# Kernel tuning notes

Hardware: AMD Instinct MI355X
Metric: run time of the kernel (lower is better)

The kernel has to match this reference:

```python
import jax, jax.numpy as jnp
import numpy as np

BN_EPS = 1e-5
DIM = 256
RED = 4
KH, KW = 3, 3


def setup_inputs() -> dict:
    key = jax.random.key(0)
    ks = jax.random.split(key, 4)
    b, c, h, w = 32, DIM, 64, 64
    hid = DIM // RED
    x = jax.random.normal(ks[0], (b, c, h, w), dtype=jnp.float32)
    # 1x1 convs are just matmuls on pooled [b, c] vectors; store as [out, in]
    w1 = jax.random.normal(ks[1], (hid, c), dtype=jnp.float32) * (1.0 / np.sqrt(c))
    bn_gamma = jnp.ones((hid,), dtype=jnp.float32)
    bn_beta = jnp.zeros((hid,), dtype=jnp.float32)
    bn_mean = jnp.zeros((hid,), dtype=jnp.float32)
    bn_var = jnp.ones((hid,), dtype=jnp.float32)
    w2 = jax.random.normal(ks[2], (c * KH * KW, hid), dtype=jnp.float32) * (1.0 / np.sqrt(hid))
    b2 = jnp.zeros((c * KH * KW,), dtype=jnp.float32)
    bias = jnp.zeros((c,), dtype=jnp.float32)
    return {"x": x, "w1": w1, "bn_gamma": bn_gamma, "bn_beta": bn_beta,
            "bn_mean": bn_mean, "bn_var": bn_var, "w2": w2, "b2": b2, "bias": bias}


def reference(x, w1, bn_gamma, bn_beta, bn_mean, bn_var, w2, b2, bias):
    b, c, h, w = x.shape
    # --- SE-style dynamic weight generation ---
    pooled = jnp.mean(x, axis=(2, 3))                      # [b, c]
    y = jnp.einsum('bc,rc->br', pooled, w1)                # conv1 (1x1, no bias)
    y = (y - bn_mean) * jax.lax.rsqrt(bn_var + BN_EPS) * bn_gamma + bn_beta
    y = jax.nn.sigmoid(y)                                  # note: relu is defined but unused in forward
    dyn = jnp.einsum('br,kr->bk', y, w2) + b2              # [b, c*KH*KW]
    dyn = dyn.reshape(b * c, 1, KH, KW)                    # per-sample depthwise kernels (OIHW)
    # --- per-sample depthwise conv via batch-as-groups trick ---
    out = jax.lax.conv_general_dilated(
        x.reshape(1, b * c, h, w), dyn,
        window_strides=(1, 1), padding=((1, 1), (1, 1)),
        feature_group_count=b * c,
        dimension_numbers=('NCHW', 'OIHW', 'NCHW'))
    out = out.reshape(b, c, h, w) + bias[None, :, None, None]
    return out
```

## Files before the change

kernel.cpp:

```cpp
#include <hip/hip_runtime.h>
#include <hip/hip_bf16.h>

#define DIM 256
#define HID 64
#define HW 4096
#define KK 2304
#define LW 73

__global__ __launch_bounds__(256) void pool_kernel(const float* __restrict__ x,
                                                   float* __restrict__ pooled) {
    int plane = blockIdx.x;
    const float4* p = (const float4*)(x + (size_t)plane * HW);
    int tid = threadIdx.x;
    float s = 0.f;
#pragma unroll
    for (int k = 0; k < 4; ++k) {
        float4 v = p[tid + k * 256];
        s += (v.x + v.y) + (v.z + v.w);
    }
#pragma unroll
    for (int off = 32; off > 0; off >>= 1) s += __shfl_down(s, off, 64);
    __shared__ float ws[4];
    int wid = tid >> 6, lane = tid & 63;
    if (lane == 0) ws[wid] = s;
    __syncthreads();
    if (tid == 0) {
        float t = (ws[0] + ws[1]) + (ws[2] + ws[3]);
        pooled[plane] = t * (1.0f / (float)HW);
    }
}

__global__ __launch_bounds__(256) void gen_kernel(const float* __restrict__ pooled,
                                                  const float* __restrict__ w1,
                                                  const float* __restrict__ gamma,
                                                  const float* __restrict__ beta,
                                                  const float* __restrict__ mean,
                                                  const float* __restrict__ var,
                                                  const float* __restrict__ w2,
                                                  const float* __restrict__ b2,
                                                  float* __restrict__ dyn) {
    int b = blockIdx.x / 9;
    int j = blockIdx.x % 9;
    int tid = threadIdx.x;
    __shared__ float sp[DIM];
    __shared__ float sig[HID];
    sp[tid] = pooled[b * DIM + tid];
    __syncthreads();
    if (tid < HID) {
        const float4* wr = (const float4*)(w1 + tid * DIM);
        const float4* s4 = (const float4*)sp;
        float acc = 0.f;
#pragma unroll
        for (int i = 0; i < DIM / 4; ++i) {
            float4 v = wr[i]; float4 u = s4[i];
            acc += v.x * u.x + v.y * u.y + v.z * u.z + v.w * u.w;
        }
        float yb = (acc - mean[tid]) * rsqrtf(var[tid] + 1e-5f) * gamma[tid] + beta[tid];
        sig[tid] = 1.0f / (1.0f + expf(-yb));
    }
    __syncthreads();
    int k = j * 256 + tid;
    const float4* wk = (const float4*)(w2 + (size_t)k * HID);
    const float4* sg4 = (const float4*)sig;
    float acc = b2[k];
#pragma unroll
    for (int i = 0; i < HID / 4; ++i) {
        float4 v = wk[i]; float4 u = sg4[i];
        acc += v.x * u.x + v.y * u.y + v.z * u.z + v.w * u.w;
    }
    dyn[b * KK + k] = acc;
}

__global__ __launch_bounds__(256) void conv_kernel(const float* __restrict__ x,
                                                   const float* __restrict__ dyn,
                                                   const float* __restrict__ bias,
                                                   float* __restrict__ out) {
    int plane = blockIdx.x;
    int c = plane & (DIM - 1);
    int b = plane >> 8;
    int tid = threadIdx.x;
    const float* xp = x + (size_t)plane * HW;
    float* op = out + (size_t)plane * HW;

    __shared__ float lds[66 * LW];

    const float4* xp4 = (const float4*)xp;
    float4 st[4];
#pragma unroll
    for (int k = 0; k < 4; ++k) st[k] = xp4[tid + k * 256];

    const float* wp = dyn + b * KK + c * 9;
    float w[9];
#pragma unroll
    for (int i = 0; i < 9; ++i) w[i] = wp[i];
    float bv = bias[c];

    for (int i = tid; i < 274; i += 256) {
        int addr;
        if (i < 73)        addr = i;
        else if (i < 146)  addr = 65 * LW + (i - 73);
        else if (i < 210)  addr = (i - 146 + 1) * LW + 3;
        else               addr = (i - 210 + 1) * LW + 68;
        lds[addr] = 0.f;
    }

#pragma unroll
    for (int k = 0; k < 4; ++k) {
        int idx = tid + k * 256;
        int row = idx >> 4;
        int col4 = idx & 15;
        float* dst = &lds[(row + 1) * LW + 4 + col4 * 4];
        dst[0] = st[k].x; dst[1] = st[k].y; dst[2] = st[k].z; dst[3] = st[k].w;
    }
    __syncthreads();

    float4* op4 = (float4*)op;
#pragma unroll
    for (int g = 0; g < 4; ++g) {
        int q = tid + g * 256;
        int row = q >> 4;
        int col0 = (q & 15) * 4;
        float s0 = bv, s1 = bv, s2 = bv, s3 = bv;
#pragma unroll
        for (int dy = 0; dy < 3; ++dy) {
            const float* r = &lds[(row + dy) * LW + 3 + col0];
            float a0 = r[0], a1 = r[1], a2 = r[2], a3 = r[3], a4 = r[4], a5 = r[5];
            float w0 = w[dy * 3 + 0], w1v = w[dy * 3 + 1], w2v = w[dy * 3 + 2];
            s0 += w0 * a0 + w1v * a1 + w2v * a2;
            s1 += w0 * a1 + w1v * a2 + w2v * a3;
            s2 += w0 * a2 + w1v * a3 + w2v * a4;
            s3 += w0 * a3 + w1v * a4 + w2v * a5;
        }
        float4 o;
        o.x = s0; o.y = s1; o.z = s2; o.w = s3;
        op4[q] = o;
    }
}

extern "C" void kernel_launch(void* const* d_in, const int* in_sizes, int n_in,
                              void* d_out, int out_size, void* d_ws, size_t ws_size,
                              hipStream_t stream) {
    const float* x     = (const float*)d_in[0];
    const float* w1    = (const float*)d_in[1];
    const float* gamma = (const float*)d_in[2];
    const float* beta  = (const float*)d_in[3];
    const float* mean  = (const float*)d_in[4];
    const float* var   = (const float*)d_in[5];
    const float* w2    = (const float*)d_in[6];
    const float* b2    = (const float*)d_in[7];
    const float* bias  = (const float*)d_in[8];
    float* out = (float*)d_out;

    float* pooled = (float*)d_ws;
    float* dyn = pooled + 8192;

    pool_kernel<<<8192, 256, 0, stream>>>(x, pooled);
    gen_kernel<<<288, 256, 0, stream>>>(pooled, w1, gamma, beta, mean, var, w2, b2, dyn);
    conv_kernel<<<8192, 256, 0, stream>>>(x, dyn, bias, out);
}
```

Measured before the change: 77.27 us.

## Fuse dynamic kernel generation into conv, skew LDS rows, register-block 4 rows per thread

Splits the weight generator so that a small kernel computes only the sigmoid hidden vector. Each conv block then computes its own 9 depthwise weights from w2 and that vector, which removes the dyn buffer round trip. The LDS tile now uses a 72-float row stride with a per-row skew to avoid bank conflicts. Each thread computes a 4x4 output patch using sliding row reuse, so it reads 6 LDS rows instead of 12. The cost is that 9 threads per block do a 64-length dot product before the barrier, and the skew adds index arithmetic.

```diff
diff --git a/kernel.cpp b/kernel.cpp
--- a/kernel.cpp
+++ b/kernel.cpp
@@ -5,7 +5,13 @@
 #define HID 64
 #define HW 4096
 #define KK 2304
-#define LW 73
+#define LW 72
+
+__device__ __forceinline__ int skew_of(int R) {
+    int r3 = R & 3;
+    int g = (r3 & 2) ? r3 : 0;
+    return ((R >> 2) + g) & 3;
+}
 
 __global__ __launch_bounds__(256) void pool_kernel(const float* __restrict__ x,
                                                    float* __restrict__ pooled) {
@@ -30,49 +36,34 @@
     }
 }
 
-__global__ __launch_bounds__(256) void gen_kernel(const float* __restrict__ pooled,
-                                                  const float* __restrict__ w1,
-                                                  const float* __restrict__ gamma,
-                                                  const float* __restrict__ beta,
-                                                  const float* __restrict__ mean,
-                                                  const float* __restrict__ var,
-                                                  const float* __restrict__ w2,
-                                                  const float* __restrict__ b2,
-                                                  float* __restrict__ dyn) {
-    int b = blockIdx.x / 9;
-    int j = blockIdx.x % 9;
-    int tid = threadIdx.x;
+__global__ __launch_bounds__(64) void sig_kernel(const float* __restrict__ pooled,
+                                                 const float* __restrict__ w1,
+                                                 const float* __restrict__ gamma,
+                                                 const float* __restrict__ beta,
+                                                 const float* __restrict__ mean,
+                                                 const float* __restrict__ var,
+                                                 float* __restrict__ sigg) {
+    int b = blockIdx.x;
+    int t = threadIdx.x;
     __shared__ float sp[DIM];
-    __shared__ float sig[HID];
-    sp[tid] = pooled[b * DIM + tid];
+    ((float4*)sp)[t] = ((const float4*)(pooled + b * DIM))[t];
     __syncthreads();
-    if (tid < HID) {
-        const float4* wr = (const float4*)(w1 + tid * DIM);
-        const float4* s4 = (const float4*)sp;
-        float acc = 0.f;
+    const float4* wr = (const float4*)(w1 + t * DIM);
+    const float4* s4 = (const float4*)sp;
+    float acc = 0.f;
 #pragma unroll
-        for (int i = 0; i < DIM / 4; ++i) {
-            float4 v = wr[i]; float4 u = s4[i];
-            acc += v.x * u.x + v.y * u.y + v.z * u.z + v.w * u.w;
-        }
-        float yb = (acc - mean[tid]) * rsqrtf(var[tid] + 1e-5f) * gamma[tid] + beta[tid];
-        sig[tid] = 1.0f / (1.0f + expf(-yb));
-    }
-    __syncthreads();
-    int k = j * 256 + tid;
-    const float4* wk = (const float4*)(w2 + (size_t)k * HID);
-    const float4* sg4 = (const float4*)sig;
-    float acc = b2[k];
-#pragma unroll
-    for (int i = 0; i < HID / 4; ++i) {
-        float4 v = wk[i]; float4 u = sg4[i];
+    for (int i = 0; i < DIM / 4; ++i) {
+        float4 v = wr[i]; float4 u = s4[i];
         acc += v.x * u.x + v.y * u.y + v.z * u.z + v.w * u.w;
     }
-    dyn[b * KK + k] = acc;
+    float yb = (acc - mean[t]) * rsqrtf(var[t] + 1e-5f) * gamma[t] + beta[t];
+    sigg[b * HID + t] = 1.0f / (1.0f + expf(-yb));
 }
 
 __global__ __launch_bounds__(256) void conv_kernel(const float* __restrict__ x,
-                                                   const float* __restrict__ dyn,
+                                                   const float* __restrict__ sigg,
+                                                   const float* __restrict__ w2,
+                                                   const float* __restrict__ b2,
                                                    const float* __restrict__ bias,
                                                    float* __restrict__ out) {
     int plane = blockIdx.x;
@@ -80,60 +71,93 @@
     int b = plane >> 8;
     int tid = threadIdx.x;
     const float* xp = x + (size_t)plane * HW;
-    float* op = out + (size_t)plane * HW;
 
     __shared__ float lds[66 * LW];
+    __shared__ float wsh[12];
 
     const float4* xp4 = (const float4*)xp;
     float4 st[4];
 #pragma unroll
     for (int k = 0; k < 4; ++k) st[k] = xp4[tid + k * 256];
 
-    const float* wp = dyn + b * KK + c * 9;
-    float w[9];
+    if (tid < 9) {
+        int kk = c * 9 + tid;
+        const float4* wk = (const float4*)(w2 + (size_t)kk * HID);
+        const float4* sg = (const float4*)(sigg + b * HID);
+        float acc = b2[kk];
 #pragma unroll
-    for (int i = 0; i < 9; ++i) w[i] = wp[i];
-    float bv = bias[c];
+        for (int i = 0; i < HID / 4; ++i) {
+            float4 v = wk[i]; float4 u = sg[i];
+            acc += v.x * u.x + v.y * u.y + v.z * u.z + v.w * u.w;
+        }
+        wsh[tid] = acc;
+    }
 
-    for (int i = tid; i < 274; i += 256) {
+    for (int i = tid; i < 272; i += 256) {
         int addr;
-        if (i < 73)        addr = i;
-        else if (i < 146)  addr = 65 * LW + (i - 73);
-        else if (i < 210)  addr = (i - 146 + 1) * LW + 3;
-        else               addr = (i - 210 + 1) * LW + 68;
+        if (i < 72)        addr = i;
+        else if (i < 144)  addr = 65 * LW + (i - 72);
+        else {
+            int z = i - 144;
+            int R = 1 + (z >> 1);
+            addr = R * LW + skew_of(R) + 3 + (z & 1) * 65;
+        }
         lds[addr] = 0.f;
     }
 
 #pragma unroll
     for (int k = 0; k < 4; ++k) {
         int idx = tid + k * 256;
-        int row = idx >> 4;
-        int col4 = idx & 15;
-        float* dst = &lds[(row + 1) * LW + 4 + col4 * 4];
+        int R = (idx >> 4) + 1;
+        int col0 = (idx & 15) * 4;
+        float* dst = &lds[R * LW + skew_of(R) + 4 + col0];
         dst[0] = st[k].x; dst[1] = st[k].y; dst[2] = st[k].z; dst[3] = st[k].w;
     }
     __syncthreads();
 
-    float4* op4 = (float4*)op;
+    float w[9];
 #pragma unroll
-    for (int g = 0; g < 4; ++g) {
-        int q = tid + g * 256;
-        int row = q >> 4;
-        int col0 = (q & 15) * 4;
-        float s0 = bv, s1 = bv, s2 = bv, s3 = bv;
+    for (int i = 0; i < 9; ++i) w[i] = wsh[i];
+    float bv = bias[c];
+
+    int u = tid >> 4, j = tid & 15;
+    float acc[4][4];
 #pragma unroll
-        for (int dy = 0; dy < 3; ++dy) {
-            const float* r = &lds[(row + dy) * LW + 3 + col0];
-            float a0 = r[0], a1 = r[1], a2 = r[2], a3 = r[3], a4 = r[4], a5 = r[5];
-            float w0 = w[dy * 3 + 0], w1v = w[dy * 3 + 1], w2v = w[dy * 3 + 2];
-            s0 += w0 * a0 + w1v * a1 + w2v * a2;
-            s1 += w0 * a1 + w1v * a2 + w2v * a3;
-            s2 += w0 * a2 + w1v * a3 + w2v * a4;
-            s3 += w0 * a3 + w1v * a4 + w2v * a5;
-        }
+    for (int m = 0; m < 4; ++m)
+#pragma unroll
+        for (int i = 0; i < 4; ++i) acc[m][i] = bv;
+
+#define CONTRIB(m, t)                                                          \
+    {                                                                          \
+        float w0 = w[(t)*3 + 0], w1v = w[(t)*3 + 1], w2v = w[(t)*3 + 2];       \
+        acc[m][0] += w0 * a0 + w1v * a1 + w2v * a2;                            \
+        acc[m][1] += w0 * a1 + w1v * a2 + w2v * a3;                            \
+        acc[m][2] += w0 * a2 + w1v * a3 + w2v * a4;                            \
+        acc[m][3] += w0 * a3 + w1v * a4 + w2v * a5;                            \
+    }
+#define READROW(d)                                                             \
+    float a0, a1, a2, a3, a4, a5;                                              \
+    {                                                                          \
+        int R = 4 * u + (d);                                                   \
+        const float* r = &lds[R * LW + skew_of(R) + 3 + 4 * j];                \
+        a0 = r[0]; a1 = r[1]; a2 = r[2]; a3 = r[3]; a4 = r[4]; a5 = r[5];      \
+    }
+
+    { READROW(0) CONTRIB(0, 0) }
+    { READROW(1) CONTRIB(0, 1) CONTRIB(1, 0) }
+    { READROW(2) CONTRIB(0, 2) CONTRIB(1, 1) CONTRIB(2, 0) }
+    { READROW(3) CONTRIB(1, 2) CONTRIB(2, 1) CONTRIB(3, 0) }
+    { READROW(4) CONTRIB(2, 2) CONTRIB(3, 1) }
+    { READROW(5) CONTRIB(3, 2) }
+#undef READROW
+#undef CONTRIB
+
+    float4* op4 = (float4*)(out + (size_t)plane * HW);
+#pragma unroll
+    for (int m = 0; m < 4; ++m) {
         float4 o;
-        o.x = s0; o.y = s1; o.z = s2; o.w = s3;
-        op4[q] = o;
+        o.x = acc[m][0]; o.y = acc[m][1]; o.z = acc[m][2]; o.w = acc[m][3];
+        op4[(4 * u + m) * 16 + j] = o;
     }
 }
 
@@ -152,9 +176,9 @@
     float* out = (float*)d_out;
 
     float* pooled = (float*)d_ws;
-    float* dyn = pooled + 8192;
+    float* sigg = pooled + 8192;
 
     pool_kernel<<<8192, 256, 0, stream>>>(x, pooled);
-    gen_kernel<<<288, 256, 0, stream>>>(pooled, w1, gamma, beta, mean, var, w2, b2, dyn);
-    conv_kernel<<<8192, 256, 0, stream>>>(x, dyn, bias, out);
+    sig_kernel<<<32, 64, 0, stream>>>(pooled, w1, gamma, beta, mean, var, sigg);
+    conv_kernel<<<8192, 256, 0, stream>>>(x, sigg, w2, b2, bias, out);
 }
```

Result: faster. 70.06 us (-9.3%).
